# Kernel optimization log

Measured on AMD Instinct MI355X. Metric: run time of the kernel, lower is better.

Reference implementation:

```python
import jax, jax.numpy as jnp
import numpy as np

N_NODES = 100000
EMB_DIM = 64
N_EDGES = 1200000
N_LAYERS = 3


def setup_inputs() -> dict:
    key = jax.random.key(0)
    k1, k2, k3 = jax.random.split(key, 3)
    embedding = jax.random.normal(k1, (N_NODES, EMB_DIM), dtype=jnp.float32)
    layer_weights = jnp.ones((N_LAYERS + 1,), dtype=jnp.float32) / (N_LAYERS + 1)
    edge_weight = jax.random.uniform(k2, (N_EDGES,), dtype=jnp.float32)
    edge_index = jax.random.randint(k3, (2, N_EDGES), 0, N_NODES, dtype=jnp.int64)
    return {"embedding": embedding, "layer_weights": layer_weights,
            "edge_weight": edge_weight, "edge_index": edge_index}


def reference(embedding, layer_weights, edge_weight, edge_index):
    # LightGCN inference (dropout off). Each LGConv applies gcn_norm
    # (no self loops) then scatter-adds norm * x[src] into dst.
    n = embedding.shape[0]
    row, col = edge_index[0], edge_index[1]  # source, target

    # gcn_norm: deg over target nodes, symmetric normalization
    deg = jax.ops.segment_sum(edge_weight, col, num_segments=n)
    dinv = jnp.where(deg > 0, jax.lax.rsqrt(deg), 0.0)
    norm = dinv[row] * edge_weight * dinv[col]  # [E]

    x = embedding
    outs = [x]
    for _ in range(N_LAYERS):
        msgs = norm[:, None] * x[row]                         # [E, D] gather
        x = jax.ops.segment_sum(msgs, col, num_segments=n)    # [N, D] scatter
        outs.append(x)

    w = jax.nn.softmax(layer_weights)                         # [L+1]
    comb = jnp.einsum('l,lnd->nd', w, jnp.stack(outs))        # weighted layer combine
    # F.normalize(dim=1), eps=1e-12
    nrm = jnp.maximum(jnp.linalg.norm(comb, axis=1, keepdims=True), 1e-12)
    return comb / nrm
```

## Files before the change

### kernel.cpp

```cpp
#include <hip/hip_runtime.h>

#define N_NODES 100000
#define EMB_DIM 64
#define N_EDGES 1200000

#define BSHIFT  7
#define BNODES  128
#define NBUCKET ((N_NODES + BNODES - 1) / BNODES)
#define CAP     2048
#define EPB     4096
#define NBLK_BIN ((N_EDGES + EPB - 1) / EPB)

#define DBINS 512
#define DNPB  1024
#define NBLK_DEG ((N_NODES + DNPB - 1) / DNPB)

#define WSCALE 32767.0f
#define WINV   (1.0f / 32767.0f)

typedef unsigned short ushort8v __attribute__((ext_vector_type(8)));

struct __align__(8) BinRec {
    unsigned meta;
    float    ew;
};

__device__ __forceinline__ unsigned short f2bf(float f) {
    unsigned u = __float_as_uint(f);
    u += 0x7FFFu + ((u >> 16) & 1u);
    return (unsigned short)(u >> 16);
}
__device__ __forceinline__ float bf2f(unsigned short h) {
    return __uint_as_float((unsigned)h << 16);
}

__global__ void init_kernel(int* __restrict__ bucket_cursor, int* __restrict__ dhist) {
    int t = threadIdx.x;
    if (t < NBUCKET) bucket_cursor[t] = t * CAP;
    if (t < DBINS)   dhist[t] = 0;
}

__global__ void bin_scatter(const int* __restrict__ row,
                            const int* __restrict__ col,
                            const float* __restrict__ ew,
                            int* __restrict__ bucket_cursor,
                            BinRec* __restrict__ binned) {
    __shared__ int hcnt[NBUCKET];
    __shared__ int hbase[NBUCKET];
    int tid = threadIdx.x;
    if (tid < NBUCKET) hcnt[tid] = 0;
    __syncthreads();
    int base = blockIdx.x * EPB;
    int end = base + EPB; if (end > N_EDGES) end = N_EDGES;
    for (int e = base + tid; e < end; e += 1024)
        atomicAdd(&hcnt[col[e] >> BSHIFT], 1);
    __syncthreads();
    if (tid < NBUCKET) {
        int c = hcnt[tid];
        hbase[tid] = c ? atomicAdd(&bucket_cursor[tid], c) : 0;
        hcnt[tid] = 0;
    }
    __syncthreads();
    for (int e = base + tid; e < end; e += 1024) {
        int c = col[e];
        int b = c >> BSHIFT;
        int rk = atomicAdd(&hcnt[b], 1);
        BinRec r;
        r.meta = (unsigned)row[e] | ((unsigned)(c & (BNODES - 1)) << 20);
        r.ew = ew[e];
        binned[hbase[b] + rk] = r;
    }
}

__global__ void bucket_scan(const int* __restrict__ cursor,
                            int* __restrict__ csr_base,
                            int* __restrict__ start) {
    __shared__ int ws[16];
    int t = threadIdx.x;
    int lane = t & 63, wid = t >> 6;
    int v = (t < NBUCKET) ? (cursor[t] - t * CAP) : 0;
    int inc = v;
    #pragma unroll
    for (int o = 1; o < 64; o <<= 1) {
        int u = __shfl_up(inc, o, 64);
        if (lane >= o) inc += u;
    }
    if (lane == 63) ws[wid] = inc;
    __syncthreads();
    int woff = 0;
    for (int w = 0; w < wid; ++w) woff += ws[w];
    if (t < NBUCKET) csr_base[t] = woff + inc - v;
    if (t == 0) start[N_NODES] = N_EDGES;
}

__global__ void bucket_build(const BinRec* __restrict__ binned,
                             const int* __restrict__ cursor,
                             const int* __restrict__ csr_base,
                             const float* __restrict__ emb,
                             float* __restrict__ dinv,
                             float* __restrict__ rdinv,
                             int* __restrict__ start,
                             unsigned* __restrict__ rec,
                             unsigned short* __restrict__ y0,
                             int* __restrict__ dhist) {
    __shared__ int   cnt[BNODES];
    __shared__ float deg[BNODES];
    __shared__ int   cur[BNODES];
    __shared__ int   dh[DBINS];
    __shared__ int   wsum[2];
    int b = blockIdx.x;
    int tid = threadIdx.x;
    if (tid < BNODES) { cnt[tid] = 0; deg[tid] = 0.0f; }
    for (int i = tid; i < DBINS; i += 256) dh[i] = 0;
    __syncthreads();
    int s = b * CAP;
    int n = cursor[b] - s;
    for (int i = tid; i < n; i += 256) {
        BinRec r = binned[s + i];
        int l = r.meta >> 20;
        atomicAdd(&cnt[l], 1);
        atomicAdd(&deg[l], r.ew);
    }
    __syncthreads();
    int lane = tid & 63, wid = tid >> 6;
    int v = (tid < BNODES) ? cnt[tid] : 0;
    int inc = v;
    #pragma unroll
    for (int o = 1; o < 64; o <<= 1) {
        int u = __shfl_up(inc, o, 64);
        if (lane >= o) inc += u;
    }
    if (tid < BNODES && lane == 63) wsum[wid] = inc;
    __syncthreads();
    if (tid < BNODES) {
        int excl = inc - v + ((wid == 1) ? wsum[0] : 0);
        int node = (b << BSHIFT) + tid;
        if (node < N_NODES) {
            int st = csr_base[b] + excl;
            start[node] = st;
            cur[tid] = st;
            float d = deg[tid];
            dinv[node]  = (d > 0.0f) ? rsqrtf(d) : 0.0f;
            rdinv[node] = (d > 0.0f) ? sqrtf(d)  : 0.0f;
            int dd = v; if (dd > DBINS - 1) dd = DBINS - 1;
            atomicAdd(&dh[dd], 1);
        } else {
            cur[tid] = 0;
        }
    }
    __syncthreads();
    for (int i = tid; i < n; i += 256) {
        BinRec r = binned[s + i];
        int l = r.meta >> 20;
        int pos = atomicAdd(&cur[l], 1);
        unsigned wq = (unsigned)rintf(r.ew * WSCALE);
        rec[pos] = ((r.meta & 0xFFFFFu) << 15) | wq;
    }
    for (int i = tid; i < DBINS; i += 256)
        if (dh[i]) atomicAdd(&dhist[i], dh[i]);
    #pragma unroll
    for (int pass = 0; pass < 4; ++pass) {
        int g = (pass * 256 + tid) * 8;
        int l = g >> 6;
        int node = (b << BSHIFT) + l;
        if (node < N_NODES) {
            float d = deg[l];
            float dn = (d > 0.0f) ? rsqrtf(d) : 0.0f;
            size_t off = (((size_t)node) << 6) + (g & 63);
            float4 a = *(const float4*)(emb + off);
            float4 bb = *(const float4*)(emb + off + 4);
            uint4 o;
            o.x = (unsigned)f2bf(dn * a.x)  | ((unsigned)f2bf(dn * a.y)  << 16);
            o.y = (unsigned)f2bf(dn * a.z)  | ((unsigned)f2bf(dn * a.w)  << 16);
            o.z = (unsigned)f2bf(dn * bb.x) | ((unsigned)f2bf(dn * bb.y) << 16);
            o.w = (unsigned)f2bf(dn * bb.z) | ((unsigned)f2bf(dn * bb.w) << 16);
            *(uint4*)(y0 + off) = o;
        }
    }
}

__global__ void deg_scan(const int* __restrict__ dhist, int* __restrict__ dcursor) {
    __shared__ int ws[8];
    int t = threadIdx.x;
    int lane = t & 63, wid = t >> 6;
    int v = dhist[t];
    int inc = v;
    #pragma unroll
    for (int o = 1; o < 64; o <<= 1) {
        int u = __shfl_up(inc, o, 64);
        if (lane >= o) inc += u;
    }
    if (lane == 63) ws[wid] = inc;
    __syncthreads();
    int woff = 0;
    for (int w = 0; w < wid; ++w) woff += ws[w];
    dcursor[t] = woff + inc - v;
}

__global__ void deg_scatter(const int* __restrict__ start,
                            int* __restrict__ dcursor,
                            int* __restrict__ perm) {
    __shared__ int h[DBINS];
    __shared__ int hb[DBINS];
    int tid = threadIdx.x;
    for (int i = tid; i < DBINS; i += 256) h[i] = 0;
    __syncthreads();
    int base = blockIdx.x * DNPB;
    int end = base + DNPB; if (end > N_NODES) end = N_NODES;
    for (int n = base + tid; n < end; n += 256) {
        int d = start[n + 1] - start[n];
        if (d > DBINS - 1) d = DBINS - 1;
        atomicAdd(&h[d], 1);
    }
    __syncthreads();
    for (int i = tid; i < DBINS; i += 256) {
        int c = h[i];
        hb[i] = c ? atomicAdd(&dcursor[i], c) : 0;
        h[i] = 0;
    }
    __syncthreads();
    for (int n = base + tid; n < end; n += 256) {
        int d = start[n + 1] - start[n];
        if (d > DBINS - 1) d = DBINS - 1;
        int rk = atomicAdd(&h[d], 1);
        perm[hb[d] + rk] = n;
    }
}

#define DECODE(v, src, w)  { src = (int)((v) >> 15); w = (float)((v) & 0x7FFFu) * WINV; }

#define GATHER_ACC(vv)                                                          \
    {   int _s; float _w; DECODE(vv, _s, _w);                                   \
        ushort8v _h = *(const ushort8v*)(yin + (((size_t)_s) << 6) + q);        \
        a0 += _w * bf2f(_h[0]); a1 += _w * bf2f(_h[1]);                         \
        a2 += _w * bf2f(_h[2]); a3 += _w * bf2f(_h[3]);                         \
        a4 += _w * bf2f(_h[4]); a5 += _w * bf2f(_h[5]);                         \
        a6 += _w * bf2f(_h[6]); a7 += _w * bf2f(_h[7]); }

__global__ void prop8_kernel(const unsigned short* __restrict__ yin,
                             unsigned short* __restrict__ yout,
                             const unsigned* __restrict__ rec,
                             const int* __restrict__ start,
                             const float* __restrict__ dinv,
                             const int* __restrict__ perm) {
    int t = blockIdx.x * blockDim.x + threadIdx.x;
    int slot = t >> 3;
    int q = (t & 7) << 3;
    if (slot >= N_NODES) return;
    int n = perm[slot];
    int s = start[n], e = start[n + 1];
    float a0 = 0.f, a1 = 0.f, a2 = 0.f, a3 = 0.f;
    float a4 = 0.f, a5 = 0.f, a6 = 0.f, a7 = 0.f;
    int j = s;
    for (; j + 8 <= e; j += 8) {
        unsigned v0 = rec[j],     v1 = rec[j + 1], v2 = rec[j + 2], v3 = rec[j + 3];
        unsigned v4 = rec[j + 4], v5 = rec[j + 5], v6 = rec[j + 6], v7 = rec[j + 7];
        const ushort8v* p0 = (const ushort8v*)(yin + (((size_t)(v0 >> 15)) << 6) + q);
        const ushort8v* p1 = (const ushort8v*)(yin + (((size_t)(v1 >> 15)) << 6) + q);
        const ushort8v* p2 = (const ushort8v*)(yin + (((size_t)(v2 >> 15)) << 6) + q);
        const ushort8v* p3 = (const ushort8v*)(yin + (((size_t)(v3 >> 15)) << 6) + q);
        const ushort8v* p4 = (const ushort8v*)(yin + (((size_t)(v4 >> 15)) << 6) + q);
        const ushort8v* p5 = (const ushort8v*)(yin + (((size_t)(v5 >> 15)) << 6) + q);
        const ushort8v* p6 = (const ushort8v*)(yin + (((size_t)(v6 >> 15)) << 6) + q);
        const ushort8v* p7 = (const ushort8v*)(yin + (((size_t)(v7 >> 15)) << 6) + q);
        ushort8v h0 = *p0, h1 = *p1, h2 = *p2, h3 = *p3;
        ushort8v h4 = *p4, h5 = *p5, h6 = *p6, h7 = *p7;
        float w0 = (float)(v0 & 0x7FFFu) * WINV, w1 = (float)(v1 & 0x7FFFu) * WINV;
        float w2 = (float)(v2 & 0x7FFFu) * WINV, w3 = (float)(v3 & 0x7FFFu) * WINV;
        float w4 = (float)(v4 & 0x7FFFu) * WINV, w5 = (float)(v5 & 0x7FFFu) * WINV;
        float w6 = (float)(v6 & 0x7FFFu) * WINV, w7 = (float)(v7 & 0x7FFFu) * WINV;
        a0 += w0*bf2f(h0[0]) + w1*bf2f(h1[0]) + w2*bf2f(h2[0]) + w3*bf2f(h3[0])
            + w4*bf2f(h4[0]) + w5*bf2f(h5[0]) + w6*bf2f(h6[0]) + w7*bf2f(h7[0]);
        a1 += w0*bf2f(h0[1]) + w1*bf2f(h1[1]) + w2*bf2f(h2[1]) + w3*bf2f(h3[1])
            + w4*bf2f(h4[1]) + w5*bf2f(h5[1]) + w6*bf2f(h6[1]) + w7*bf2f(h7[1]);
        a2 += w0*bf2f(h0[2]) + w1*bf2f(h1[2]) + w2*bf2f(h2[2]) + w3*bf2f(h3[2])
            + w4*bf2f(h4[2]) + w5*bf2f(h5[2]) + w6*bf2f(h6[2]) + w7*bf2f(h7[2]);
        a3 += w0*bf2f(h0[3]) + w1*bf2f(h1[3]) + w2*bf2f(h2[3]) + w3*bf2f(h3[3])
            + w4*bf2f(h4[3]) + w5*bf2f(h5[3]) + w6*bf2f(h6[3]) + w7*bf2f(h7[3]);
        a4 += w0*bf2f(h0[4]) + w1*bf2f(h1[4]) + w2*bf2f(h2[4]) + w3*bf2f(h3[4])
            + w4*bf2f(h4[4]) + w5*bf2f(h5[4]) + w6*bf2f(h6[4]) + w7*bf2f(h7[4]);
        a5 += w0*bf2f(h0[5]) + w1*bf2f(h1[5]) + w2*bf2f(h2[5]) + w3*bf2f(h3[5])
            + w4*bf2f(h4[5]) + w5*bf2f(h5[5]) + w6*bf2f(h6[5]) + w7*bf2f(h7[5]);
        a6 += w0*bf2f(h0[6]) + w1*bf2f(h1[6]) + w2*bf2f(h2[6]) + w3*bf2f(h3[6])
            + w4*bf2f(h4[6]) + w5*bf2f(h5[6]) + w6*bf2f(h6[6]) + w7*bf2f(h7[6]);
        a7 += w0*bf2f(h0[7]) + w1*bf2f(h1[7]) + w2*bf2f(h2[7]) + w3*bf2f(h3[7])
            + w4*bf2f(h4[7]) + w5*bf2f(h5[7]) + w6*bf2f(h6[7]) + w7*bf2f(h7[7]);
    }
    if (j + 4 <= e) {
        unsigned v0 = rec[j], v1 = rec[j + 1], v2 = rec[j + 2], v3 = rec[j + 3];
        ushort8v h0 = *(const ushort8v*)(yin + (((size_t)(v0 >> 15)) << 6) + q);
        ushort8v h1 = *(const ushort8v*)(yin + (((size_t)(v1 >> 15)) << 6) + q);
        ushort8v h2 = *(const ushort8v*)(yin + (((size_t)(v2 >> 15)) << 6) + q);
        ushort8v h3 = *(const ushort8v*)(yin + (((size_t)(v3 >> 15)) << 6) + q);
        float w0 = (float)(v0 & 0x7FFFu) * WINV, w1 = (float)(v1 & 0x7FFFu) * WINV;
        float w2 = (float)(v2 & 0x7FFFu) * WINV, w3 = (float)(v3 & 0x7FFFu) * WINV;
        a0 += w0*bf2f(h0[0]) + w1*bf2f(h1[0]) + w2*bf2f(h2[0]) + w3*bf2f(h3[0]);
        a1 += w0*bf2f(h0[1]) + w1*bf2f(h1[1]) + w2*bf2f(h2[1]) + w3*bf2f(h3[1]);
        a2 += w0*bf2f(h0[2]) + w1*bf2f(h1[2]) + w2*bf2f(h2[2]) + w3*bf2f(h3[2]);
        a3 += w0*bf2f(h0[3]) + w1*bf2f(h1[3]) + w2*bf2f(h2[3]) + w3*bf2f(h3[3]);
        a4 += w0*bf2f(h0[4]) + w1*bf2f(h1[4]) + w2*bf2f(h2[4]) + w3*bf2f(h3[4]);
        a5 += w0*bf2f(h0[5]) + w1*bf2f(h1[5]) + w2*bf2f(h2[5]) + w3*bf2f(h3[5]);
        a6 += w0*bf2f(h0[6]) + w1*bf2f(h1[6]) + w2*bf2f(h2[6]) + w3*bf2f(h3[6]);
        a7 += w0*bf2f(h0[7]) + w1*bf2f(h1[7]) + w2*bf2f(h2[7]) + w3*bf2f(h3[7]);
        j += 4;
    }
    for (; j < e; ++j) GATHER_ACC(rec[j]);
    float dn = dinv[n];
    float dn2 = dn * dn;
    uint4 o;
    o.x = (unsigned)f2bf(dn2 * a0) | ((unsigned)f2bf(dn2 * a1) << 16);
    o.y = (unsigned)f2bf(dn2 * a2) | ((unsigned)f2bf(dn2 * a3) << 16);
    o.z = (unsigned)f2bf(dn2 * a4) | ((unsigned)f2bf(dn2 * a5) << 16);
    o.w = (unsigned)f2bf(dn2 * a6) | ((unsigned)f2bf(dn2 * a7) << 16);
    *(uint4*)(yout + (((size_t)n) << 6) + q) = o;
}

__global__ void prop8_combine_kernel(const unsigned short* __restrict__ yin,
                                     const unsigned short* __restrict__ y0h,
                                     const unsigned short* __restrict__ y1h,
                                     const float* __restrict__ emb,
                                     const unsigned* __restrict__ rec,
                                     const int* __restrict__ start,
                                     const float* __restrict__ dinv,
                                     const float* __restrict__ rdinv,
                                     const float* __restrict__ lw,
                                     const int* __restrict__ perm,
                                     float* __restrict__ out) {
    int t = blockIdx.x * blockDim.x + threadIdx.x;
    int slot = t >> 3;
    int q = (t & 7) << 3;
    if (slot >= N_NODES) return;
    int n = perm[slot];
    int s = start[n], e = start[n + 1];
    float a0 = 0.f, a1 = 0.f, a2 = 0.f, a3 = 0.f;
    float a4 = 0.f, a5 = 0.f, a6 = 0.f, a7 = 0.f;
    int j = s;
    for (; j + 8 <= e; j += 8) {
        unsigned v0 = rec[j],     v1 = rec[j + 1], v2 = rec[j + 2], v3 = rec[j + 3];
        unsigned v4 = rec[j + 4], v5 = rec[j + 5], v6 = rec[j + 6], v7 = rec[j + 7];
        ushort8v h0 = *(const ushort8v*)(yin + (((size_t)(v0 >> 15)) << 6) + q);
        ushort8v h1 = *(const ushort8v*)(yin + (((size_t)(v1 >> 15)) << 6) + q);
        ushort8v h2 = *(const ushort8v*)(yin + (((size_t)(v2 >> 15)) << 6) + q);
        ushort8v h3 = *(const ushort8v*)(yin + (((size_t)(v3 >> 15)) << 6) + q);
        ushort8v h4 = *(const ushort8v*)(yin + (((size_t)(v4 >> 15)) << 6) + q);
        ushort8v h5 = *(const ushort8v*)(yin + (((size_t)(v5 >> 15)) << 6) + q);
        ushort8v h6 = *(const ushort8v*)(yin + (((size_t)(v6 >> 15)) << 6) + q);
        ushort8v h7 = *(const ushort8v*)(yin + (((size_t)(v7 >> 15)) << 6) + q);
        float w0 = (float)(v0 & 0x7FFFu) * WINV, w1 = (float)(v1 & 0x7FFFu) * WINV;
        float w2 = (float)(v2 & 0x7FFFu) * WINV, w3 = (float)(v3 & 0x7FFFu) * WINV;
        float w4 = (float)(v4 & 0x7FFFu) * WINV, w5 = (float)(v5 & 0x7FFFu) * WINV;
        float w6 = (float)(v6 & 0x7FFFu) * WINV, w7 = (float)(v7 & 0x7FFFu) * WINV;
        a0 += w0*bf2f(h0[0]) + w1*bf2f(h1[0]) + w2*bf2f(h2[0]) + w3*bf2f(h3[0])
            + w4*bf2f(h4[0]) + w5*bf2f(h5[0]) + w6*bf2f(h6[0]) + w7*bf2f(h7[0]);
        a1 += w0*bf2f(h0[1]) + w1*bf2f(h1[1]) + w2*bf2f(h2[1]) + w3*bf2f(h3[1])
            + w4*bf2f(h4[1]) + w5*bf2f(h5[1]) + w6*bf2f(h6[1]) + w7*bf2f(h7[1]);
        a2 += w0*bf2f(h0[2]) + w1*bf2f(h1[2]) + w2*bf2f(h2[2]) + w3*bf2f(h3[2])
            + w4*bf2f(h4[2]) + w5*bf2f(h5[2]) + w6*bf2f(h6[2]) + w7*bf2f(h7[2]);
        a3 += w0*bf2f(h0[3]) + w1*bf2f(h1[3]) + w2*bf2f(h2[3]) + w3*bf2f(h3[3])
            + w4*bf2f(h4[3]) + w5*bf2f(h5[3]) + w6*bf2f(h6[3]) + w7*bf2f(h7[3]);
        a4 += w0*bf2f(h0[4]) + w1*bf2f(h1[4]) + w2*bf2f(h2[4]) + w3*bf2f(h3[4])
            + w4*bf2f(h4[4]) + w5*bf2f(h5[4]) + w6*bf2f(h6[4]) + w7*bf2f(h7[4]);
        a5 += w0*bf2f(h0[5]) + w1*bf2f(h1[5]) + w2*bf2f(h2[5]) + w3*bf2f(h3[5])
            + w4*bf2f(h4[5]) + w5*bf2f(h5[5]) + w6*bf2f(h6[5]) + w7*bf2f(h7[5]);
        a6 += w0*bf2f(h0[6]) + w1*bf2f(h1[6]) + w2*bf2f(h2[6]) + w3*bf2f(h3[6])
            + w4*bf2f(h4[6]) + w5*bf2f(h5[6]) + w6*bf2f(h6[6]) + w7*bf2f(h7[6]);
        a7 += w0*bf2f(h0[7]) + w1*bf2f(h1[7]) + w2*bf2f(h2[7]) + w3*bf2f(h3[7])
            + w4*bf2f(h4[7]) + w5*bf2f(h5[7]) + w6*bf2f(h6[7]) + w7*bf2f(h7[7]);
    }
    if (j + 4 <= e) {
        unsigned v0 = rec[j], v1 = rec[j + 1], v2 = rec[j + 2], v3 = rec[j + 3];
        ushort8v h0 = *(const ushort8v*)(yin + (((size_t)(v0 >> 15)) << 6) + q);
        ushort8v h1 = *(const ushort8v*)(yin + (((size_t)(v1 >> 15)) << 6) + q);
        ushort8v h2 = *(const ushort8v*)(yin + (((size_t)(v2 >> 15)) << 6) + q);
        ushort8v h3 = *(const ushort8v*)(yin + (((size_t)(v3 >> 15)) << 6) + q);
        float w0 = (float)(v0 & 0x7FFFu) * WINV, w1 = (float)(v1 & 0x7FFFu) * WINV;
        float w2 = (float)(v2 & 0x7FFFu) * WINV, w3 = (float)(v3 & 0x7FFFu) * WINV;
        a0 += w0*bf2f(h0[0]) + w1*bf2f(h1[0]) + w2*bf2f(h2[0]) + w3*bf2f(h3[0]);
        a1 += w0*bf2f(h0[1]) + w1*bf2f(h1[1]) + w2*bf2f(h2[1]) + w3*bf2f(h3[1]);
        a2 += w0*bf2f(h0[2]) + w1*bf2f(h1[2]) + w2*bf2f(h2[2]) + w3*bf2f(h3[2]);
        a3 += w0*bf2f(h0[3]) + w1*bf2f(h1[3]) + w2*bf2f(h2[3]) + w3*bf2f(h3[3]);
        a4 += w0*bf2f(h0[4]) + w1*bf2f(h1[4]) + w2*bf2f(h2[4]) + w3*bf2f(h3[4]);
        a5 += w0*bf2f(h0[5]) + w1*bf2f(h1[5]) + w2*bf2f(h2[5]) + w3*bf2f(h3[5]);
        a6 += w0*bf2f(h0[6]) + w1*bf2f(h1[6]) + w2*bf2f(h2[6]) + w3*bf2f(h3[6]);
        a7 += w0*bf2f(h0[7]) + w1*bf2f(h1[7]) + w2*bf2f(h2[7]) + w3*bf2f(h3[7]);
        j += 4;
    }
    { const unsigned short* yin_ = yin;
      for (; j < e; ++j) { const unsigned short* yin2 = yin_;
        unsigned vv = rec[j];
        int _s = (int)(vv >> 15); float _w = (float)(vv & 0x7FFFu) * WINV;
        ushort8v _h = *(const ushort8v*)(yin2 + (((size_t)_s) << 6) + q);
        a0 += _w * bf2f(_h[0]); a1 += _w * bf2f(_h[1]);
        a2 += _w * bf2f(_h[2]); a3 += _w * bf2f(_h[3]);
        a4 += _w * bf2f(_h[4]); a5 += _w * bf2f(_h[5]);
        a6 += _w * bf2f(_h[6]); a7 += _w * bf2f(_h[7]); } }

    float dn = dinv[n];
    float rn = rdinv[n];

    float w0 = lw[0], w1 = lw[1], w2 = lw[2], w3 = lw[3];
    float m = fmaxf(fmaxf(w0, w1), fmaxf(w2, w3));
    float e0 = expf(w0 - m), e1 = expf(w1 - m), e2 = expf(w2 - m), e3 = expf(w3 - m);
    float inv_s = 1.0f / (e0 + e1 + e2 + e3);
    float c0 = e0 * rn, c1 = e1 * rn, c2 = e2 * rn, c3 = e3 * dn;

    size_t off = (((size_t)n) << 6) + q;
    float v0, v1, v2, v3, v4, v5, v6, v7;
    if (rn != 0.0f) {
        ushort8v h0v = *(const ushort8v*)(y0h + off);
        ushort8v h1v = *(const ushort8v*)(y1h + off);
        ushort8v h2v = *(const ushort8v*)(yin + off);
        v0 = (c0 * bf2f(h0v[0]) + c1 * bf2f(h1v[0]) + c2 * bf2f(h2v[0]) + c3 * a0) * inv_s;
        v1 = (c0 * bf2f(h0v[1]) + c1 * bf2f(h1v[1]) + c2 * bf2f(h2v[1]) + c3 * a1) * inv_s;
        v2 = (c0 * bf2f(h0v[2]) + c1 * bf2f(h1v[2]) + c2 * bf2f(h2v[2]) + c3 * a2) * inv_s;
        v3 = (c0 * bf2f(h0v[3]) + c1 * bf2f(h1v[3]) + c2 * bf2f(h2v[3]) + c3 * a3) * inv_s;
        v4 = (c0 * bf2f(h0v[4]) + c1 * bf2f(h1v[4]) + c2 * bf2f(h2v[4]) + c3 * a4) * inv_s;
        v5 = (c0 * bf2f(h0v[5]) + c1 * bf2f(h1v[5]) + c2 * bf2f(h2v[5]) + c3 * a5) * inv_s;
        v6 = (c0 * bf2f(h0v[6]) + c1 * bf2f(h1v[6]) + c2 * bf2f(h2v[6]) + c3 * a6) * inv_s;
        v7 = (c0 * bf2f(h0v[7]) + c1 * bf2f(h1v[7]) + c2 * bf2f(h2v[7]) + c3 * a7) * inv_s;
    } else {
        float4 xa = *(const float4*)(emb + off);
        float4 xb = *(const float4*)(emb + off + 4);
        float c = e0 * inv_s;
        v0 = c * xa.x; v1 = c * xa.y; v2 = c * xa.z; v3 = c * xa.w;
        v4 = c * xb.x; v5 = c * xb.y; v6 = c * xb.z; v7 = c * xb.w;
    }

    float sq = v0*v0 + v1*v1 + v2*v2 + v3*v3 + v4*v4 + v5*v5 + v6*v6 + v7*v7;
    #pragma unroll
    for (int o = 1; o < 8; o <<= 1) sq += __shfl_xor(sq, o, 64);
    float nrm = fmaxf(sqrtf(sq), 1e-12f);
    float inv_n = 1.0f / nrm;

    float4 oa, ob;
    oa.x = v0 * inv_n; oa.y = v1 * inv_n; oa.z = v2 * inv_n; oa.w = v3 * inv_n;
    ob.x = v4 * inv_n; ob.y = v5 * inv_n; ob.z = v6 * inv_n; ob.w = v7 * inv_n;
    *(float4*)(out + off) = oa;
    *(float4*)(out + off + 4) = ob;
}

extern "C" void kernel_launch(void* const* d_in, const int* in_sizes, int n_in,
                              void* d_out, int out_size, void* d_ws, size_t ws_size,
                              hipStream_t stream) {
    const float* emb = (const float*)d_in[0];
    const float* lw  = (const float*)d_in[1];
    const float* ew  = (const float*)d_in[2];
    const int*   ei  = (const int*)d_in[3];
    const int* row = ei;
    const int* col = ei + N_EDGES;
    float* out = (float*)d_out;

    char* p = (char*)d_ws;
    BinRec*  binned = (BinRec*)p;               p += (size_t)NBUCKET * CAP * sizeof(BinRec);
    unsigned* rec   = (unsigned*)p;             p += (size_t)N_EDGES * 4;
    unsigned short* y0h = (unsigned short*)p;   p += (size_t)N_NODES * EMB_DIM * 2;
    unsigned short* y1h = (unsigned short*)p;   p += (size_t)N_NODES * EMB_DIM * 2;
    unsigned short* y2h = (unsigned short*)p;   p += (size_t)N_NODES * EMB_DIM * 2;
    float* dinv  = (float*)p;                   p += (size_t)N_NODES * 4;
    float* rdinv = (float*)p;                   p += (size_t)N_NODES * 4;
    int*   startA= (int*)p;                     p += (size_t)(N_NODES + 8) * 4;
    int*   perm  = (int*)p;                     p += (size_t)N_NODES * 4;
    int*   csr_base      = (int*)p;             p += (size_t)NBUCKET * 4;
    int*   bucket_cursor = (int*)p;             p += (size_t)NBUCKET * 4;
    int*   dhist   = (int*)p;                   p += (size_t)DBINS * 4;
    int*   dcursor = (int*)p;                   p += (size_t)DBINS * 4;

    const int B = 256;

    init_kernel<<<1, 1024, 0, stream>>>(bucket_cursor, dhist);
    bin_scatter<<<NBLK_BIN, 1024, 0, stream>>>(row, col, ew, bucket_cursor, binned);
    bucket_scan<<<1, 1024, 0, stream>>>(bucket_cursor, csr_base, startA);
    bucket_build<<<NBUCKET, B, 0, stream>>>(binned, bucket_cursor, csr_base, emb,
                                            dinv, rdinv, startA, rec, y0h, dhist);
    deg_scan<<<1, DBINS, 0, stream>>>(dhist, dcursor);
    deg_scatter<<<NBLK_DEG, B, 0, stream>>>(startA, dcursor, perm);

    long pt = (long)N_NODES * 8;
    int pgrid = (int)((pt + B - 1) / B);
    prop8_kernel<<<pgrid, B, 0, stream>>>(y0h, y1h, rec, startA, dinv, perm);
    prop8_kernel<<<pgrid, B, 0, stream>>>(y1h, y2h, rec, startA, dinv, perm);
    prop8_combine_kernel<<<pgrid, B, 0, stream>>>(y2h, y0h, y1h, emb, rec, startA,
                                                  dinv, rdinv, lw, perm, out);
}
```

Measured before the change: 150.8 us.

## Process two nodes per 8-lane group in propagation and cache bin records in LDS

Each 8-thread group now handles two degree-sorted nodes at once, interleaving 4-edge gathers from both so more independent loads are in flight per thread, and the grid is halved. Separately, bucket_build stages its binned records in shared memory so the second pass reads LDS instead of re-reading global memory. The cost is more registers per thread (two accumulator sets), which can lower occupancy, plus 16 KB of LDS per bucket_build block. The inner unroll also drops from 8 to 4 edges per node.

Measured after the change: 165.5 us. +9.7%, slower.

```diff
diff --git a/kernel.cpp b/kernel.cpp
--- a/kernel.cpp
+++ b/kernel.cpp
@@ -103,6 +103,7 @@
                              unsigned* __restrict__ rec,
                              unsigned short* __restrict__ y0,
                              int* __restrict__ dhist) {
+    __shared__ BinRec lbin[CAP];
     __shared__ int   cnt[BNODES];
     __shared__ float deg[BNODES];
     __shared__ int   cur[BNODES];
@@ -117,6 +118,7 @@
     int n = cursor[b] - s;
     for (int i = tid; i < n; i += 256) {
         BinRec r = binned[s + i];
+        lbin[i] = r;
         int l = r.meta >> 20;
         atomicAdd(&cnt[l], 1);
         atomicAdd(&deg[l], r.ew);
@@ -150,7 +152,7 @@
     }
     __syncthreads();
     for (int i = tid; i < n; i += 256) {
-        BinRec r = binned[s + i];
+        BinRec r = lbin[i];
         int l = r.meta >> 20;
         int pos = atomicAdd(&cur[l], 1);
         unsigned wq = (unsigned)rintf(r.ew * WSCALE);
@@ -227,189 +229,116 @@
     }
 }
 
-#define DECODE(v, src, w)  { src = (int)((v) >> 15); w = (float)((v) & 0x7FFFu) * WINV; }
-
-#define GATHER_ACC(vv)                                                          \
-    {   int _s; float _w; DECODE(vv, _s, _w);                                   \
-        ushort8v _h = *(const ushort8v*)(yin + (((size_t)_s) << 6) + q);        \
-        a0 += _w * bf2f(_h[0]); a1 += _w * bf2f(_h[1]);                         \
-        a2 += _w * bf2f(_h[2]); a3 += _w * bf2f(_h[3]);                         \
-        a4 += _w * bf2f(_h[4]); a5 += _w * bf2f(_h[5]);                         \
-        a6 += _w * bf2f(_h[6]); a7 += _w * bf2f(_h[7]); }
-
-__global__ void prop8_kernel(const unsigned short* __restrict__ yin,
-                             unsigned short* __restrict__ yout,
-                             const unsigned* __restrict__ rec,
-                             const int* __restrict__ start,
-                             const float* __restrict__ dinv,
-                             const int* __restrict__ perm) {
+__device__ __forceinline__ void gather4(const unsigned* __restrict__ rec, int j,
+                                        const unsigned short* __restrict__ yin, int q,
+                                        float& a0, float& a1, float& a2, float& a3,
+                                        float& a4, float& a5, float& a6, float& a7) {
+    unsigned v0 = rec[j], v1 = rec[j + 1], v2 = rec[j + 2], v3 = rec[j + 3];
+    ushort8v h0 = *(const ushort8v*)(yin + (((size_t)(v0 >> 15)) << 6) + q);
+    ushort8v h1 = *(const ushort8v*)(yin + (((size_t)(v1 >> 15)) << 6) + q);
+    ushort8v h2 = *(const ushort8v*)(yin + (((size_t)(v2 >> 15)) << 6) + q);
+    ushort8v h3 = *(const ushort8v*)(yin + (((size_t)(v3 >> 15)) << 6) + q);
+    float w0 = (float)(v0 & 0x7FFFu) * WINV, w1 = (float)(v1 & 0x7FFFu) * WINV;
+    float w2 = (float)(v2 & 0x7FFFu) * WINV, w3 = (float)(v3 & 0x7FFFu) * WINV;
+    a0 += w0*bf2f(h0[0]) + w1*bf2f(h1[0]) + w2*bf2f(h2[0]) + w3*bf2f(h3[0]);
+    a1 += w0*bf2f(h0[1]) + w1*bf2f(h1[1]) + w2*bf2f(h2[1]) + w3*bf2f(h3[1]);
+    a2 += w0*bf2f(h0[2]) + w1*bf2f(h1[2]) + w2*bf2f(h2[2]) + w3*bf2f(h3[2]);
+    a3 += w0*bf2f(h0[3]) + w1*bf2f(h1[3]) + w2*bf2f(h2[3]) + w3*bf2f(h3[3]);
+    a4 += w0*bf2f(h0[4]) + w1*bf2f(h1[4]) + w2*bf2f(h2[4]) + w3*bf2f(h3[4]);
+    a5 += w0*bf2f(h0[5]) + w1*bf2f(h1[5]) + w2*bf2f(h2[5]) + w3*bf2f(h3[5]);
+    a6 += w0*bf2f(h0[6]) + w1*bf2f(h1[6]) + w2*bf2f(h2[6]) + w3*bf2f(h3[6]);
+    a7 += w0*bf2f(h0[7]) + w1*bf2f(h1[7]) + w2*bf2f(h2[7]) + w3*bf2f(h3[7]);
+}
+
+__device__ __forceinline__ void gather1(const unsigned* __restrict__ rec, int j,
+                                        const unsigned short* __restrict__ yin, int q,
+                                        float& a0, float& a1, float& a2, float& a3,
+                                        float& a4, float& a5, float& a6, float& a7) {
+    unsigned v = rec[j];
+    ushort8v h = *(const ushort8v*)(yin + (((size_t)(v >> 15)) << 6) + q);
+    float w = (float)(v & 0x7FFFu) * WINV;
+    a0 += w * bf2f(h[0]); a1 += w * bf2f(h[1]);
+    a2 += w * bf2f(h[2]); a3 += w * bf2f(h[3]);
+    a4 += w * bf2f(h[4]); a5 += w * bf2f(h[5]);
+    a6 += w * bf2f(h[6]); a7 += w * bf2f(h[7]);
+}
+
+#define ACCA aA0, aA1, aA2, aA3, aA4, aA5, aA6, aA7
+#define ACCB aB0, aB1, aB2, aB3, aB4, aB5, aB6, aB7
+
+__global__ void prop8x2_kernel(const unsigned short* __restrict__ yin,
+                               unsigned short* __restrict__ yout,
+                               const unsigned* __restrict__ rec,
+                               const int* __restrict__ start,
+                               const float* __restrict__ dinv,
+                               const int* __restrict__ perm) {
     int t = blockIdx.x * blockDim.x + threadIdx.x;
-    int slot = t >> 3;
+    int g = t >> 3;
     int q = (t & 7) << 3;
-    if (slot >= N_NODES) return;
-    int n = perm[slot];
-    int s = start[n], e = start[n + 1];
-    float a0 = 0.f, a1 = 0.f, a2 = 0.f, a3 = 0.f;
-    float a4 = 0.f, a5 = 0.f, a6 = 0.f, a7 = 0.f;
-    int j = s;
-    for (; j + 8 <= e; j += 8) {
-        unsigned v0 = rec[j],     v1 = rec[j + 1], v2 = rec[j + 2], v3 = rec[j + 3];
-        unsigned v4 = rec[j + 4], v5 = rec[j + 5], v6 = rec[j + 6], v7 = rec[j + 7];
-        const ushort8v* p0 = (const ushort8v*)(yin + (((size_t)(v0 >> 15)) << 6) + q);
-        const ushort8v* p1 = (const ushort8v*)(yin + (((size_t)(v1 >> 15)) << 6) + q);
-        const ushort8v* p2 = (const ushort8v*)(yin + (((size_t)(v2 >> 15)) << 6) + q);
-        const ushort8v* p3 = (const ushort8v*)(yin + (((size_t)(v3 >> 15)) << 6) + q);
-        const ushort8v* p4 = (const ushort8v*)(yin + (((size_t)(v4 >> 15)) << 6) + q);
-        const ushort8v* p5 = (const ushort8v*)(yin + (((size_t)(v5 >> 15)) << 6) + q);
-        const ushort8v* p6 = (const ushort8v*)(yin + (((size_t)(v6 >> 15)) << 6) + q);
-        const ushort8v* p7 = (const ushort8v*)(yin + (((size_t)(v7 >> 15)) << 6) + q);
-        ushort8v h0 = *p0, h1 = *p1, h2 = *p2, h3 = *p3;
-        ushort8v h4 = *p4, h5 = *p5, h6 = *p6, h7 = *p7;
-        float w0 = (float)(v0 & 0x7FFFu) * WINV, w1 = (float)(v1 & 0x7FFFu) * WINV;
-        float w2 = (float)(v2 & 0x7FFFu) * WINV, w3 = (float)(v3 & 0x7FFFu) * WINV;
-        float w4 = (float)(v4 & 0x7FFFu) * WINV, w5 = (float)(v5 & 0x7FFFu) * WINV;
-        float w6 = (float)(v6 & 0x7FFFu) * WINV, w7 = (float)(v7 & 0x7FFFu) * WINV;
-        a0 += w0*bf2f(h0[0]) + w1*bf2f(h1[0]) + w2*bf2f(h2[0]) + w3*bf2f(h3[0])
-            + w4*bf2f(h4[0]) + w5*bf2f(h5[0]) + w6*bf2f(h6[0]) + w7*bf2f(h7[0]);
-        a1 += w0*bf2f(h0[1]) + w1*bf2f(h1[1]) + w2*bf2f(h2[1]) + w3*bf2f(h3[1])
-            + w4*bf2f(h4[1]) + w5*bf2f(h5[1]) + w6*bf2f(h6[1]) + w7*bf2f(h7[1]);
-        a2 += w0*bf2f(h0[2]) + w1*bf2f(h1[2]) + w2*bf2f(h2[2]) + w3*bf2f(h3[2])
-            + w4*bf2f(h4[2]) + w5*bf2f(h5[2]) + w6*bf2f(h6[2]) + w7*bf2f(h7[2]);
-        a3 += w0*bf2f(h0[3]) + w1*bf2f(h1[3]) + w2*bf2f(h2[3]) + w3*bf2f(h3[3])
-            + w4*bf2f(h4[3]) + w5*bf2f(h5[3]) + w6*bf2f(h6[3]) + w7*bf2f(h7[3]);
-        a4 += w0*bf2f(h0[4]) + w1*bf2f(h1[4]) + w2*bf2f(h2[4]) + w3*bf2f(h3[4])
-            + w4*bf2f(h4[4]) + w5*bf2f(h5[4]) + w6*bf2f(h6[4]) + w7*bf2f(h7[4]);
-        a5 += w0*bf2f(h0[5]) + w1*bf2f(h1[5]) + w2*bf2f(h2[5]) + w3*bf2f(h3[5])
-            + w4*bf2f(h4[5]) + w5*bf2f(h5[5]) + w6*bf2f(h6[5]) + w7*bf2f(h7[5]);
-        a6 += w0*bf2f(h0[6]) + w1*bf2f(h1[6]) + w2*bf2f(h2[6]) + w3*bf2f(h3[6])
-            + w4*bf2f(h4[6]) + w5*bf2f(h5[6]) + w6*bf2f(h6[6]) + w7*bf2f(h7[6]);
-        a7 += w0*bf2f(h0[7]) + w1*bf2f(h1[7]) + w2*bf2f(h2[7]) + w3*bf2f(h3[7])
-            + w4*bf2f(h4[7]) + w5*bf2f(h5[7]) + w6*bf2f(h6[7]) + w7*bf2f(h7[7]);
-    }
-    if (j + 4 <= e) {
-        unsigned v0 = rec[j], v1 = rec[j + 1], v2 = rec[j + 2], v3 = rec[j + 3];
-        ushort8v h0 = *(const ushort8v*)(yin + (((size_t)(v0 >> 15)) << 6) + q);
-        ushort8v h1 = *(const ushort8v*)(yin + (((size_t)(v1 >> 15)) << 6) + q);
-        ushort8v h2 = *(const ushort8v*)(yin + (((size_t)(v2 >> 15)) << 6) + q);
-        ushort8v h3 = *(const ushort8v*)(yin + (((size_t)(v3 >> 15)) << 6) + q);
-        float w0 = (float)(v0 & 0x7FFFu) * WINV, w1 = (float)(v1 & 0x7FFFu) * WINV;
-        float w2 = (float)(v2 & 0x7FFFu) * WINV, w3 = (float)(v3 & 0x7FFFu) * WINV;
-        a0 += w0*bf2f(h0[0]) + w1*bf2f(h1[0]) + w2*bf2f(h2[0]) + w3*bf2f(h3[0]);
-        a1 += w0*bf2f(h0[1]) + w1*bf2f(h1[1]) + w2*bf2f(h2[1]) + w3*bf2f(h3[1]);
-        a2 += w0*bf2f(h0[2]) + w1*bf2f(h1[2]) + w2*bf2f(h2[2]) + w3*bf2f(h3[2]);
-        a3 += w0*bf2f(h0[3]) + w1*bf2f(h1[3]) + w2*bf2f(h2[3]) + w3*bf2f(h3[3]);
-        a4 += w0*bf2f(h0[4]) + w1*bf2f(h1[4]) + w2*bf2f(h2[4]) + w3*bf2f(h3[4]);
-        a5 += w0*bf2f(h0[5]) + w1*bf2f(h1[5]) + w2*bf2f(h2[5]) + w3*bf2f(h3[5]);
-        a6 += w0*bf2f(h0[6]) + w1*bf2f(h1[6]) + w2*bf2f(h2[6]) + w3*bf2f(h3[6]);
-        a7 += w0*bf2f(h0[7]) + w1*bf2f(h1[7]) + w2*bf2f(h2[7]) + w3*bf2f(h3[7]);
-        j += 4;
-    }
-    for (; j < e; ++j) GATHER_ACC(rec[j]);
-    float dn = dinv[n];
-    float dn2 = dn * dn;
-    uint4 o;
-    o.x = (unsigned)f2bf(dn2 * a0) | ((unsigned)f2bf(dn2 * a1) << 16);
-    o.y = (unsigned)f2bf(dn2 * a2) | ((unsigned)f2bf(dn2 * a3) << 16);
-    o.z = (unsigned)f2bf(dn2 * a4) | ((unsigned)f2bf(dn2 * a5) << 16);
-    o.w = (unsigned)f2bf(dn2 * a6) | ((unsigned)f2bf(dn2 * a7) << 16);
-    *(uint4*)(yout + (((size_t)n) << 6) + q) = o;
-}
-
-__global__ void prop8_combine_kernel(const unsigned short* __restrict__ yin,
-                                     const unsigned short* __restrict__ y0h,
-                                     const unsigned short* __restrict__ y1h,
-                                     const float* __restrict__ emb,
-                                     const unsigned* __restrict__ rec,
-                                     const int* __restrict__ start,
-                                     const float* __restrict__ dinv,
-                                     const float* __restrict__ rdinv,
-                                     const float* __restrict__ lw,
-                                     const int* __restrict__ perm,
-                                     float* __restrict__ out) {
-    int t = blockIdx.x * blockDim.x + threadIdx.x;
-    int slot = t >> 3;
-    int q = (t & 7) << 3;
-    if (slot >= N_NODES) return;
-    int n = perm[slot];
-    int s = start[n], e = start[n + 1];
-    float a0 = 0.f, a1 = 0.f, a2 = 0.f, a3 = 0.f;
-    float a4 = 0.f, a5 = 0.f, a6 = 0.f, a7 = 0.f;
-    int j = s;
-    for (; j + 8 <= e; j += 8) {
-        unsigned v0 = rec[j],     v1 = rec[j + 1], v2 = rec[j + 2], v3 = rec[j + 3];
-        unsigned v4 = rec[j + 4], v5 = rec[j + 5], v6 = rec[j + 6], v7 = rec[j + 7];
-        ushort8v h0 = *(const ushort8v*)(yin + (((size_t)(v0 >> 15)) << 6) + q);
-        ushort8v h1 = *(const ushort8v*)(yin + (((size_t)(v1 >> 15)) << 6) + q);
-        ushort8v h2 = *(const ushort8v*)(yin + (((size_t)(v2 >> 15)) << 6) + q);
-        ushort8v h3 = *(const ushort8v*)(yin + (((size_t)(v3 >> 15)) << 6) + q);
-        ushort8v h4 = *(const ushort8v*)(yin + (((size_t)(v4 >> 15)) << 6) + q);
-        ushort8v h5 = *(const ushort8v*)(yin + (((size_t)(v5 >> 15)) << 6) + q);
-        ushort8v h6 = *(const ushort8v*)(yin + (((size_t)(v6 >> 15)) << 6) + q);
-        ushort8v h7 = *(const ushort8v*)(yin + (((size_t)(v7 >> 15)) << 6) + q);
-        float w0 = (float)(v0 & 0x7FFFu) * WINV, w1 = (float)(v1 & 0x7FFFu) * WINV;
-        float w2 = (float)(v2 & 0x7FFFu) * WINV, w3 = (float)(v3 & 0x7FFFu) * WINV;
-        float w4 = (float)(v4 & 0x7FFFu) * WINV, w5 = (float)(v5 & 0x7FFFu) * WINV;
-        float w6 = (float)(v6 & 0x7FFFu) * WINV, w7 = (float)(v7 & 0x7FFFu) * WINV;
-        a0 += w0*bf2f(h0[0]) + w1*bf2f(h1[0]) + w2*bf2f(h2[0]) + w3*bf2f(h3[0])
-            + w4*bf2f(h4[0]) + w5*bf2f(h5[0]) + w6*bf2f(h6[0]) + w7*bf2f(h7[0]);
-        a1 += w0*bf2f(h0[1]) + w1*bf2f(h1[1]) + w2*bf2f(h2[1]) + w3*bf2f(h3[1])
-            + w4*bf2f(h4[1]) + w5*bf2f(h5[1]) + w6*bf2f(h6[1]) + w7*bf2f(h7[1]);
-        a2 += w0*bf2f(h0[2]) + w1*bf2f(h1[2]) + w2*bf2f(h2[2]) + w3*bf2f(h3[2])
-            + w4*bf2f(h4[2]) + w5*bf2f(h5[2]) + w6*bf2f(h6[2]) + w7*bf2f(h7[2]);
-        a3 += w0*bf2f(h0[3]) + w1*bf2f(h1[3]) + w2*bf2f(h2[3]) + w3*bf2f(h3[3])
-            + w4*bf2f(h4[3]) + w5*bf2f(h5[3]) + w6*bf2f(h6[3]) + w7*bf2f(h7[3]);
-        a4 += w0*bf2f(h0[4]) + w1*bf2f(h1[4]) + w2*bf2f(h2[4]) + w3*bf2f(h3[4])
-            + w4*bf2f(h4[4]) + w5*bf2f(h5[4]) + w6*bf2f(h6[4]) + w7*bf2f(h7[4]);
-        a5 += w0*bf2f(h0[5]) + w1*bf2f(h1[5]) + w2*bf2f(h2[5]) + w3*bf2f(h3[5])
-            + w4*bf2f(h4[5]) + w5*bf2f(h5[5]) + w6*bf2f(h6[5]) + w7*bf2f(h7[5]);
-        a6 += w0*bf2f(h0[6]) + w1*bf2f(h1[6]) + w2*bf2f(h2[6]) + w3*bf2f(h3[6])
-            + w4*bf2f(h4[6]) + w5*bf2f(h5[6]) + w6*bf2f(h6[6]) + w7*bf2f(h7[6]);
-        a7 += w0*bf2f(h0[7]) + w1*bf2f(h1[7]) + w2*bf2f(h2[7]) + w3*bf2f(h3[7])
-            + w4*bf2f(h4[7]) + w5*bf2f(h5[7]) + w6*bf2f(h6[7]) + w7*bf2f(h7[7]);
-    }
-    if (j + 4 <= e) {
-        unsigned v0 = rec[j], v1 = rec[j + 1], v2 = rec[j + 2], v3 = rec[j + 3];
-        ushort8v h0 = *(const ushort8v*)(yin + (((size_t)(v0 >> 15)) << 6) + q);
-        ushort8v h1 = *(const ushort8v*)(yin + (((size_t)(v1 >> 15)) << 6) + q);
-        ushort8v h2 = *(const ushort8v*)(yin + (((size_t)(v2 >> 15)) << 6) + q);
-        ushort8v h3 = *(const ushort8v*)(yin + (((size_t)(v3 >> 15)) << 6) + q);
-        float w0 = (float)(v0 & 0x7FFFu) * WINV, w1 = (float)(v1 & 0x7FFFu) * WINV;
-        float w2 = (float)(v2 & 0x7FFFu) * WINV, w3 = (float)(v3 & 0x7FFFu) * WINV;
-        a0 += w0*bf2f(h0[0]) + w1*bf2f(h1[0]) + w2*bf2f(h2[0]) + w3*bf2f(h3[0]);
-        a1 += w0*bf2f(h0[1]) + w1*bf2f(h1[1]) + w2*bf2f(h2[1]) + w3*bf2f(h3[1]);
-        a2 += w0*bf2f(h0[2]) + w1*bf2f(h1[2]) + w2*bf2f(h2[2]) + w3*bf2f(h3[2]);
-        a3 += w0*bf2f(h0[3]) + w1*bf2f(h1[3]) + w2*bf2f(h2[3]) + w3*bf2f(h3[3]);
-        a4 += w0*bf2f(h0[4]) + w1*bf2f(h1[4]) + w2*bf2f(h2[4]) + w3*bf2f(h3[4]);
-        a5 += w0*bf2f(h0[5]) + w1*bf2f(h1[5]) + w2*bf2f(h2[5]) + w3*bf2f(h3[5]);
-        a6 += w0*bf2f(h0[6]) + w1*bf2f(h1[6]) + w2*bf2f(h2[6]) + w3*bf2f(h3[6]);
-        a7 += w0*bf2f(h0[7]) + w1*bf2f(h1[7]) + w2*bf2f(h2[7]) + w3*bf2f(h3[7]);
-        j += 4;
-    }
-    { const unsigned short* yin_ = yin;
-      for (; j < e; ++j) { const unsigned short* yin2 = yin_;
-        unsigned vv = rec[j];
-        int _s = (int)(vv >> 15); float _w = (float)(vv & 0x7FFFu) * WINV;
-        ushort8v _h = *(const ushort8v*)(yin2 + (((size_t)_s) << 6) + q);
-        a0 += _w * bf2f(_h[0]); a1 += _w * bf2f(_h[1]);
-        a2 += _w * bf2f(_h[2]); a3 += _w * bf2f(_h[3]);
-        a4 += _w * bf2f(_h[4]); a5 += _w * bf2f(_h[5]);
-        a6 += _w * bf2f(_h[6]); a7 += _w * bf2f(_h[7]); } }
-
+    int sA = g * 2, sB = g * 2 + 1;
+    if (sA >= N_NODES) return;
+    int nA = perm[sA];
+    int nB = (sB < N_NODES) ? perm[sB] : -1;
+    int jA = start[nA], eA = start[nA + 1];
+    int jB = 0, eB = 0;
+    if (nB >= 0) { jB = start[nB]; eB = start[nB + 1]; }
+
+    float aA0 = 0.f, aA1 = 0.f, aA2 = 0.f, aA3 = 0.f, aA4 = 0.f, aA5 = 0.f, aA6 = 0.f, aA7 = 0.f;
+    float aB0 = 0.f, aB1 = 0.f, aB2 = 0.f, aB3 = 0.f, aB4 = 0.f, aB5 = 0.f, aB6 = 0.f, aB7 = 0.f;
+
+    while (jA + 4 <= eA && jB + 4 <= eB) {
+        gather4(rec, jA, yin, q, ACCA);
+        gather4(rec, jB, yin, q, ACCB);
+        jA += 4; jB += 4;
+    }
+    for (; jA + 4 <= eA; jA += 4) gather4(rec, jA, yin, q, ACCA);
+    for (; jB + 4 <= eB; jB += 4) gather4(rec, jB, yin, q, ACCB);
+    for (; jA < eA; ++jA) gather1(rec, jA, yin, q, ACCA);
+    for (; jB < eB; ++jB) gather1(rec, jB, yin, q, ACCB);
+
+    {
+        float dn = dinv[nA];
+        float dn2 = dn * dn;
+        uint4 o;
+        o.x = (unsigned)f2bf(dn2 * aA0) | ((unsigned)f2bf(dn2 * aA1) << 16);
+        o.y = (unsigned)f2bf(dn2 * aA2) | ((unsigned)f2bf(dn2 * aA3) << 16);
+        o.z = (unsigned)f2bf(dn2 * aA4) | ((unsigned)f2bf(dn2 * aA5) << 16);
+        o.w = (unsigned)f2bf(dn2 * aA6) | ((unsigned)f2bf(dn2 * aA7) << 16);
+        *(uint4*)(yout + (((size_t)nA) << 6) + q) = o;
+    }
+    if (nB >= 0) {
+        float dn = dinv[nB];
+        float dn2 = dn * dn;
+        uint4 o;
+        o.x = (unsigned)f2bf(dn2 * aB0) | ((unsigned)f2bf(dn2 * aB1) << 16);
+        o.y = (unsigned)f2bf(dn2 * aB2) | ((unsigned)f2bf(dn2 * aB3) << 16);
+        o.z = (unsigned)f2bf(dn2 * aB4) | ((unsigned)f2bf(dn2 * aB5) << 16);
+        o.w = (unsigned)f2bf(dn2 * aB6) | ((unsigned)f2bf(dn2 * aB7) << 16);
+        *(uint4*)(yout + (((size_t)nB) << 6) + q) = o;
+    }
+}
+
+__device__ __forceinline__ void combine_store(int n, int q,
+                                              float a0, float a1, float a2, float a3,
+                                              float a4, float a5, float a6, float a7,
+                                              const unsigned short* __restrict__ y0h,
+                                              const unsigned short* __restrict__ y1h,
+                                              const unsigned short* __restrict__ y2h,
+                                              const float* __restrict__ emb,
+                                              const float* __restrict__ dinv,
+                                              const float* __restrict__ rdinv,
+                                              float e0, float e1, float e2, float e3,
+                                              float inv_s,
+                                              float* __restrict__ out) {
     float dn = dinv[n];
     float rn = rdinv[n];
-
-    float w0 = lw[0], w1 = lw[1], w2 = lw[2], w3 = lw[3];
-    float m = fmaxf(fmaxf(w0, w1), fmaxf(w2, w3));
-    float e0 = expf(w0 - m), e1 = expf(w1 - m), e2 = expf(w2 - m), e3 = expf(w3 - m);
-    float inv_s = 1.0f / (e0 + e1 + e2 + e3);
     float c0 = e0 * rn, c1 = e1 * rn, c2 = e2 * rn, c3 = e3 * dn;
-
     size_t off = (((size_t)n) << 6) + q;
     float v0, v1, v2, v3, v4, v5, v6, v7;
     if (rn != 0.0f) {
         ushort8v h0v = *(const ushort8v*)(y0h + off);
         ushort8v h1v = *(const ushort8v*)(y1h + off);
-        ushort8v h2v = *(const ushort8v*)(yin + off);
+        ushort8v h2v = *(const ushort8v*)(y2h + off);
         v0 = (c0 * bf2f(h0v[0]) + c1 * bf2f(h1v[0]) + c2 * bf2f(h2v[0]) + c3 * a0) * inv_s;
         v1 = (c0 * bf2f(h0v[1]) + c1 * bf2f(h1v[1]) + c2 * bf2f(h2v[1]) + c3 * a1) * inv_s;
         v2 = (c0 * bf2f(h0v[2]) + c1 * bf2f(h1v[2]) + c2 * bf2f(h2v[2]) + c3 * a2) * inv_s;
@@ -425,18 +354,61 @@
         v0 = c * xa.x; v1 = c * xa.y; v2 = c * xa.z; v3 = c * xa.w;
         v4 = c * xb.x; v5 = c * xb.y; v6 = c * xb.z; v7 = c * xb.w;
     }
-
     float sq = v0*v0 + v1*v1 + v2*v2 + v3*v3 + v4*v4 + v5*v5 + v6*v6 + v7*v7;
     #pragma unroll
     for (int o = 1; o < 8; o <<= 1) sq += __shfl_xor(sq, o, 64);
     float nrm = fmaxf(sqrtf(sq), 1e-12f);
     float inv_n = 1.0f / nrm;
-
     float4 oa, ob;
     oa.x = v0 * inv_n; oa.y = v1 * inv_n; oa.z = v2 * inv_n; oa.w = v3 * inv_n;
     ob.x = v4 * inv_n; ob.y = v5 * inv_n; ob.z = v6 * inv_n; ob.w = v7 * inv_n;
     *(float4*)(out + off) = oa;
     *(float4*)(out + off + 4) = ob;
+}
+
+__global__ void prop8x2_combine_kernel(const unsigned short* __restrict__ yin,
+                                       const unsigned short* __restrict__ y0h,
+                                       const unsigned short* __restrict__ y1h,
+                                       const float* __restrict__ emb,
+                                       const unsigned* __restrict__ rec,
+                                       const int* __restrict__ start,
+                                       const float* __restrict__ dinv,
+                                       const float* __restrict__ rdinv,
+                                       const float* __restrict__ lw,
+                                       const int* __restrict__ perm,
+                                       float* __restrict__ out) {
+    int t = blockIdx.x * blockDim.x + threadIdx.x;
+    int g = t >> 3;
+    int q = (t & 7) << 3;
+    int sA = g * 2, sB = g * 2 + 1;
+    if (sA >= N_NODES) return;
+    int nA = perm[sA];
+    int nB = (sB < N_NODES) ? perm[sB] : -1;
+    int jA = start[nA], eA = start[nA + 1];
+    int jB = 0, eB = 0;
+    if (nB >= 0) { jB = start[nB]; eB = start[nB + 1]; }
+
+    float aA0 = 0.f, aA1 = 0.f, aA2 = 0.f, aA3 = 0.f, aA4 = 0.f, aA5 = 0.f, aA6 = 0.f, aA7 = 0.f;
+    float aB0 = 0.f, aB1 = 0.f, aB2 = 0.f, aB3 = 0.f, aB4 = 0.f, aB5 = 0.f, aB6 = 0.f, aB7 = 0.f;
+
+    while (jA + 4 <= eA && jB + 4 <= eB) {
+        gather4(rec, jA, yin, q, ACCA);
+        gather4(rec, jB, yin, q, ACCB);
+        jA += 4; jB += 4;
+    }
+    for (; jA + 4 <= eA; jA += 4) gather4(rec, jA, yin, q, ACCA);
+    for (; jB + 4 <= eB; jB += 4) gather4(rec, jB, yin, q, ACCB);
+    for (; jA < eA; ++jA) gather1(rec, jA, yin, q, ACCA);
+    for (; jB < eB; ++jB) gather1(rec, jB, yin, q, ACCB);
+
+    float w0 = lw[0], w1 = lw[1], w2 = lw[2], w3 = lw[3];
+    float m = fmaxf(fmaxf(w0, w1), fmaxf(w2, w3));
+    float e0 = expf(w0 - m), e1 = expf(w1 - m), e2 = expf(w2 - m), e3 = expf(w3 - m);
+    float inv_s = 1.0f / (e0 + e1 + e2 + e3);
+
+    combine_store(nA, q, ACCA, y0h, y1h, yin, emb, dinv, rdinv, e0, e1, e2, e3, inv_s, out);
+    if (nB >= 0)
+        combine_store(nB, q, ACCB, y0h, y1h, yin, emb, dinv, rdinv, e0, e1, e2, e3, inv_s, out);
 }
 
 extern "C" void kernel_launch(void* const* d_in, const int* in_sizes, int n_in,
@@ -475,10 +447,10 @@
     deg_scan<<<1, DBINS, 0, stream>>>(dhist, dcursor);
     deg_scatter<<<NBLK_DEG, B, 0, stream>>>(startA, dcursor, perm);
 
-    long pt = (long)N_NODES * 8;
+    long pt = (long)((N_NODES + 1) / 2) * 8;
     int pgrid = (int)((pt + B - 1) / B);
-    prop8_kernel<<<pgrid, B, 0, stream>>>(y0h, y1h, rec, startA, dinv, perm);
-    prop8_kernel<<<pgrid, B, 0, stream>>>(y1h, y2h, rec, startA, dinv, perm);
-    prop8_combine_kernel<<<pgrid, B, 0, stream>>>(y2h, y0h, y1h, emb, rec, startA,
-                                                  dinv, rdinv, lw, perm, out);
-}
+    prop8x2_kernel<<<pgrid, B, 0, stream>>>(y0h, y1h, rec, startA, dinv, perm);
+    prop8x2_kernel<<<pgrid, B, 0, stream>>>(y1h, y2h, rec, startA, dinv, perm);
+    prop8x2_combine_kernel<<<pgrid, B, 0, stream>>>(y2h, y0h, y1h, emb, rec, startA,
+                                                    dinv, rdinv, lw, perm, out);
+}
```
